# Kernel optimization log

Hardware: AMD Instinct MI355X
Metric: run time of the kernel (lower is better)

Reference implementation:

```python
import jax, jax.numpy as jnp
import numpy as np

EMBED_DIM = 512
NUM_HEADS = 8
QKV_DIM = 64
MS_HIDDEN = 16
COST_DIMS = 1
SCORES_DIMS = COST_DIMS + 1  # dot-product score + cost-mat score


def setup_inputs() -> dict:
    key = jax.random.key(0)
    ks = jax.random.split(key, 12)
    B, R, C = 8, 256, 256
    row_emb = jax.random.normal(ks[0], (B, R, EMBED_DIM), dtype=jnp.float32)
    col_emb = jax.random.normal(ks[1], (B, C, EMBED_DIM), dtype=jnp.float32)
    cost_mat = jax.random.uniform(ks[2], (B, R, C, COST_DIMS), dtype=jnp.float32)
    attn_mask = jax.random.randint(ks[3], (B, R, C), 0, 2).astype(jnp.bool_)
    # learned params (stored [in, out]; torch Linear applies x @ W.T)
    s = 1.0 / np.sqrt(EMBED_DIM)
    Wq = jax.random.uniform(ks[4], (EMBED_DIM, NUM_HEADS * QKV_DIM), minval=-s, maxval=s)
    Wk = jax.random.uniform(ks[5], (EMBED_DIM, NUM_HEADS * QKV_DIM), minval=-s, maxval=s)
    Wv = jax.random.uniform(ks[6], (EMBED_DIM, NUM_HEADS * QKV_DIM), minval=-s, maxval=s)
    Wo = jax.random.uniform(ks[7], (EMBED_DIM, EMBED_DIM), minval=-s, maxval=s)
    m1 = np.sqrt(1.0 / SCORES_DIMS)
    m2 = np.sqrt(1.0 / MS_HIDDEN)
    W1 = jax.random.uniform(ks[8], (SCORES_DIMS * NUM_HEADS, MS_HIDDEN * NUM_HEADS), minval=-m1, maxval=m1)
    W2 = jax.random.uniform(ks[9], (MS_HIDDEN * NUM_HEADS, NUM_HEADS), minval=-m2, maxval=m2)
    alpha = jnp.ones((1, NUM_HEADS, 1, 1, 1), dtype=jnp.float32)
    return {"row_emb": row_emb, "col_emb": col_emb, "cost_mat": cost_mat,
            "attn_mask": attn_mask, "Wq": Wq, "Wk": Wk, "Wv": Wv, "Wo": Wo,
            "W1": W1, "W2": W2, "alpha": alpha}


def reference(row_emb, col_emb, cost_mat, attn_mask, Wq, Wk, Wv, Wo, W1, W2, alpha):
    B, R, E = row_emb.shape
    C = col_emb.shape[1]
    H, D = NUM_HEADS, QKV_DIM
    norm = 1.0 / jnp.sqrt(jnp.asarray(D, row_emb.dtype))
    # projections -> (b, h, s, d)
    q = (row_emb @ Wq).reshape(B, R, H, D).transpose(0, 2, 1, 3)
    k = (col_emb @ Wk).reshape(B, C, H, D).transpose(0, 2, 1, 3)
    v = (col_emb @ Wv).reshape(B, C, H, D).transpose(0, 2, 1, 3)
    dot = norm * jnp.einsum('bhrd,bhcd->bhrc', q, k)  # (B,H,R,C)
    # mixed-score MLP: concat dot score with alpha-scaled cost-mat score
    cm = alpha * cost_mat[:, None]                    # (B,H,R,C,COST_DIMS)
    scores = jnp.concatenate([dot[..., None], cm], axis=-1)  # (B,H,R,C,S)
    s = scores.transpose(0, 2, 3, 1, 4).reshape(B, R, C, H * SCORES_DIMS)
    mixed = jax.nn.relu(s @ W1) @ W2                  # (B,R,C,H)
    logits = mixed.transpose(0, 3, 1, 2)              # (B,H,R,C)
    # masked softmax (rows fully masked -> zero weights)
    mask = attn_mask[:, None]                         # (B,1,R,C)
    all_masked = jnp.all(mask, axis=-1, keepdims=True)
    logits = jnp.where(mask, -jnp.inf, logits)
    weights = jax.nn.softmax(logits, axis=-1)
    weights = jnp.where(all_masked, 0.0, weights)
    out = jnp.einsum('bhrc,bhcd->bhrd', weights, v)   # (B,H,R,D)
    out = out.transpose(0, 2, 1, 3).reshape(B, R, H * D)
    return out @ Wo
```

## Files before the change

### kernel.cpp

```cpp
#include <hip/hip_runtime.h>
#include <hip/hip_bf16.h>

#define B_ 8
#define R_ 256
#define C_ 256
#define H_ 8
#define D_ 64

typedef __attribute__((ext_vector_type(8))) short s8v;
typedef __attribute__((ext_vector_type(4))) short s4v;
typedef __attribute__((ext_vector_type(4))) float f4v;

static __device__ __forceinline__ unsigned short f2b(float x) {
    __hip_bfloat16 h = __float2bfloat16(x);
    return *reinterpret_cast<unsigned short*>(&h);
}
static __device__ __forceinline__ float b2f(unsigned short u) {
    union { unsigned int i; float f; } c;
    c.i = (unsigned int)u << 16;
    return c.f;
}

__global__ __launch_bounds__(256) void prep(
    const float* __restrict__ re, const float* __restrict__ ce,
    const float* __restrict__ W1, const float* __restrict__ W2,
    const float* __restrict__ alpha,
    const float* __restrict__ Wq, const float* __restrict__ Wk,
    const float* __restrict__ Wv, const float* __restrict__ Wo,
    unsigned short* __restrict__ reb, unsigned short* __restrict__ ceb,
    unsigned short* __restrict__ w1af, unsigned short* __restrict__ w2af,
    unsigned short* __restrict__ wqt, unsigned short* __restrict__ wkt,
    unsigned short* __restrict__ wvt, unsigned short* __restrict__ wot)
{
    __shared__ unsigned short ldsT[64][68];
    if (blockIdx.x >= 2048) {
        const int bb = blockIdx.x - 2048;
        const int which = bb >> 6;
        const float* W = which == 0 ? Wq : which == 1 ? Wk : which == 2 ? Wv : Wo;
        unsigned short* WT = which == 0 ? wqt : which == 1 ? wkt : which == 2 ? wvt : wot;
        const int k0 = (bb & 7) * 64;
        const int n0 = ((bb >> 3) & 7) * 64;
        const int tt = threadIdx.x;
        const int rn = tt & 15;
        const int rk = tt >> 4;
        #pragma unroll
        for (int i = 0; i < 4; ++i) {
            const int kk = rk + 16 * i;
            const float4 v = *(const float4*)&W[(size_t)(k0 + kk) * 512 + n0 + rn * 4];
            ldsT[rn * 4 + 0][kk] = f2b(v.x);
            ldsT[rn * 4 + 1][kk] = f2b(v.y);
            ldsT[rn * 4 + 2][kk] = f2b(v.z);
            ldsT[rn * 4 + 3][kk] = f2b(v.w);
        }
        __syncthreads();
        #pragma unroll
        for (int i = 0; i < 4; ++i) {
            const int nn = rk + 16 * i;
            const s4v r = *(const s4v*)&ldsT[nn][rn * 4];
            *(s4v*)&WT[(size_t)(n0 + nn) * 512 + k0 + rn * 4] = r;
        }
        return;
    }

    const int t = blockIdx.x * 256 + threadIdx.x;
    {
        float2 v = *(const float2*)&re[(size_t)t * 2];
        reb[t * 2]     = f2b(v.x);
        reb[t * 2 + 1] = f2b(v.y);
        float2 w = *(const float2*)&ce[(size_t)t * 2];
        ceb[t * 2]     = f2b(w.x);
        ceb[t * 2 + 1] = f2b(w.y);
    }
    if (blockIdx.x == 0) {
        const int l = threadIdx.x;
        for (int q = 0; q < 16; ++q) {
            const int idx = l * 16 + q;
            const int kk = idx & 7, lane = (idx >> 3) & 63, n = idx >> 9;
            const int j = n * 16 + (lane & 15);
            const int s = 8 * (lane >> 4) + kk;
            float val = 0.f;
            if (s < 16) {
                val = W1[(2 * (s >> 1)) * 128 + j];
            } else if (s < 18) {
                for (int h = 0; h < 8; ++h)
                    val += alpha[h] * W1[(2 * h + 1) * 128 + j];
            }
            w1af[idx] = f2b(val);
        }
        for (int q = 0; q < 8; ++q) {
            const int idx = l * 8 + q;
            const int kk = idx & 7, lane = (idx >> 3) & 63, kc = idx >> 9;
            const int h = lane & 15, g = lane >> 4;
            const int phi = 16 * (2 * kc + (kk >> 2)) + 4 * g + (kk & 3);
            w2af[idx] = f2b(h < 8 ? W2[phi * 8 + h] : 0.f);
        }
    }
}

__global__ __launch_bounds__(256) void gemm_qkv(
    const unsigned short* __restrict__ reb, const unsigned short* __restrict__ ceb,
    const unsigned short* __restrict__ wqt, const unsigned short* __restrict__ wkt,
    const unsigned short* __restrict__ wvt,
    unsigned short* __restrict__ Qb, unsigned short* __restrict__ Kb,
    unsigned short* __restrict__ VT)
{
    const int z = blockIdx.z;
    const unsigned short* A;
    const unsigned short* Bm;
    int Ar0, Br0;
    if (z == 0)      { A = reb; Bm = wqt; Ar0 = blockIdx.x * 64; Br0 = blockIdx.y * 64; }
    else if (z == 1) { A = ceb; Bm = wkt; Ar0 = blockIdx.x * 64; Br0 = blockIdx.y * 64; }
    else             { A = wvt; Bm = ceb; Ar0 = blockIdx.y * 64; Br0 = blockIdx.x * 64; }

    const int t = threadIdx.x, lane = t & 63, wave = t >> 6;
    const int row0 = Ar0 + (wave >> 1) * 32;
    const int col0 = Br0 + (wave & 1) * 32;
    const int lr = lane & 15, ko = (lane >> 4) * 8;

    const unsigned short* Ap0 = A + (size_t)(row0 + lr) * 512 + ko;
    const unsigned short* Ap1 = Ap0 + 16 * 512;
    const unsigned short* Bp0 = Bm + (size_t)(col0 + lr) * 512 + ko;
    const unsigned short* Bp1 = Bp0 + 16 * 512;

    f4v acc[2][2] = {};
    #pragma unroll 4
    for (int k0 = 0; k0 < 512; k0 += 32) {
        s8v a0 = *(const s8v*)(Ap0 + k0);
        s8v a1 = *(const s8v*)(Ap1 + k0);
        s8v b0 = *(const s8v*)(Bp0 + k0);
        s8v b1 = *(const s8v*)(Bp1 + k0);
        acc[0][0] = __builtin_amdgcn_mfma_f32_16x16x32_bf16(a0, b0, acc[0][0], 0, 0, 0);
        acc[0][1] = __builtin_amdgcn_mfma_f32_16x16x32_bf16(a0, b1, acc[0][1], 0, 0, 0);
        acc[1][0] = __builtin_amdgcn_mfma_f32_16x16x32_bf16(a1, b0, acc[1][0], 0, 0, 0);
        acc[1][1] = __builtin_amdgcn_mfma_f32_16x16x32_bf16(a1, b1, acc[1][1], 0, 0, 0);
    }

    const float sc = (z == 0) ? 0.125f : 1.0f;
    const int rbase = (lane >> 4) * 4;
    #pragma unroll
    for (int i = 0; i < 2; ++i)
        #pragma unroll
        for (int j = 0; j < 2; ++j)
            #pragma unroll
            for (int reg = 0; reg < 4; ++reg) {
                const int rowIdx = row0 + i * 16 + rbase + reg;
                const int colIdx = col0 + j * 16 + lr;
                const unsigned short v = f2b(acc[i][j][reg] * sc);
                if (z == 0) {
                    Qb[(size_t)rowIdx * 512 + colIdx] = v;
                } else if (z == 1) {
                    const int b = rowIdx >> 8, c = rowIdx & 255;
                    const int h = colIdx >> 6, d = colIdx & 63;
                    Kb[(((size_t)b * 8 + h) * 256 + c) * 64 + d] = v;
                } else {
                    const int h = rowIdx >> 6, d = rowIdx & 63;
                    const int b = colIdx >> 8, c = colIdx & 255;
                    VT[(((size_t)b * 8 + h) * 64 + d) * 256 + c] = v;
                }
            }
}

__global__ __launch_bounds__(256) void gemm_out(
    const unsigned short* __restrict__ OHb, const unsigned short* __restrict__ wot,
    float* __restrict__ out)
{
    const int t = threadIdx.x, lane = t & 63, wave = t >> 6;
    const int row0 = blockIdx.x * 32 + (wave & 1) * 16;
    const int col0 = blockIdx.y * 64 + (wave >> 1) * 32;
    const int lr = lane & 15, ko = (lane >> 4) * 8;

    const unsigned short* Ap0 = OHb + (size_t)(row0 + lr) * 512 + ko;
    const unsigned short* Bp0 = wot + (size_t)(col0 + lr) * 512 + ko;
    const unsigned short* Bp1 = Bp0 + 16 * 512;

    f4v acc[2] = {};
    #pragma unroll 4
    for (int k0 = 0; k0 < 512; k0 += 32) {
        s8v a0 = *(const s8v*)(Ap0 + k0);
        s8v b0 = *(const s8v*)(Bp0 + k0);
        s8v b1 = *(const s8v*)(Bp1 + k0);
        acc[0] = __builtin_amdgcn_mfma_f32_16x16x32_bf16(a0, b0, acc[0], 0, 0, 0);
        acc[1] = __builtin_amdgcn_mfma_f32_16x16x32_bf16(a0, b1, acc[1], 0, 0, 0);
    }

    const int rbase = (lane >> 4) * 4;
    #pragma unroll
    for (int j = 0; j < 2; ++j)
        #pragma unroll
        for (int reg = 0; reg < 4; ++reg)
            out[(size_t)(row0 + rbase + reg) * 512 + col0 + j * 16 + lr] = acc[j][reg];
}

__global__ __launch_bounds__(512, 2) void attn_fused(
    const unsigned short* __restrict__ Qb,
    const unsigned short* __restrict__ Kb,
    const unsigned short* __restrict__ VT,
    const float* __restrict__ cost,
    const int* __restrict__ mask,
    const unsigned short* __restrict__ w1af,
    const unsigned short* __restrict__ w2af,
    unsigned short* __restrict__ OHb)
{
    __shared__ unsigned short dotb[4][256][24];
    __shared__ unsigned short w_t3[8][4][264];
    __shared__ unsigned short ws1[4096];
    __shared__ unsigned short ws2[2048];

    const int t    = threadIdx.x;
    const int lane = t & 63;
    const int w    = t >> 6;
    const int li   = lane & 15;
    const int g    = lane >> 4;
    const int b    = blockIdx.y;
    const int r0   = blockIdx.x * 4;

    ((s8v*)ws1)[t] = ((const s8v*)w1af)[t];
    if (t < 256) ((s8v*)ws2)[t] = ((const s8v*)w2af)[t];

    const int rB  = w & 3;
    const int ct0 = (w >> 2) * 8;
    float costv[8];
    {
        const float* costRow = cost + ((size_t)b * R_ + r0 + rB) * 256;
        #pragma unroll
        for (int i = 0; i < 8; ++i)
            costv[i] = costRow[(ct0 + i) * 16 + li];
    }
    int4 mk4[4];
    #pragma unroll
    for (int p = 0; p < 4; ++p) {
        const int idx = w * 4 + p;
        mk4[p] = *(const int4*)&mask[((size_t)b * R_ + r0 + (idx >> 3)) * 256 + lane * 4];
    }

    {
        const int rr = lane & 3;
        const int ko = g * 8;
        const unsigned short* Qp = Qb + ((size_t)b * R_ + r0 + rr) * 512 + w * 64 + ko;
        const s8v a0 = *(const s8v*)Qp;
        const s8v a1 = *(const s8v*)(Qp + 32);
        const unsigned short* Kp = Kb + (((size_t)b * 8 + w) * 256) * 64;
        #pragma unroll
        for (int ct = 0; ct < 16; ++ct) {
            const unsigned short* Bp = Kp + (size_t)(ct * 16 + li) * 64 + ko;
            const s8v b0 = *(const s8v*)Bp;
            const s8v b1v = *(const s8v*)(Bp + 32);
            f4v acc = __builtin_amdgcn_mfma_f32_16x16x32_bf16(a0, b0, (f4v){0.f,0.f,0.f,0.f}, 0, 0, 0);
            acc = __builtin_amdgcn_mfma_f32_16x16x32_bf16(a1, b1v, acc, 0, 0, 0);
            if (lane < 16) {
                const int c = ct * 16 + lane;
                #pragma unroll
                for (int reg = 0; reg < 4; ++reg) {
                    const float x = acc[reg];
                    const unsigned short hi = f2b(x);
                    const unsigned short lo = f2b(x - b2f(hi));
                    *(unsigned int*)&dotb[reg][c][2 * w] =
                        (unsigned int)hi | ((unsigned int)lo << 16);
                }
            }
        }
    }
    __syncthreads();

    {
        #pragma unroll
        for (int i = 0; i < 8; ++i) {
            const int c = (ct0 + i) * 16 + li;
            s8v b1;
            {
                const s8v t0 = *(const s8v*)&dotb[rB][c][(g & 1) * 8];
                const float cv = costv[i];
                const unsigned short chi = f2b(cv);
                const unsigned short clo = f2b(cv - b2f(chi));
                if (g < 2) {
                    b1 = t0;
                } else if (g == 2) {
                    s8v bc = {0, 0, 0, 0, 0, 0, 0, 0};
                    bc[0] = (short)chi; bc[1] = (short)clo;
                    b1 = bc;
                } else {
                    s8v bz = {0, 0, 0, 0, 0, 0, 0, 0};
                    b1 = bz;
                }
            }
            unsigned int pk[16];
            #pragma unroll
            for (int n = 0; n < 8; ++n) {
                const s8v w1A = *(const s8v*)&ws1[(n * 64 + lane) * 8];
                f4v acc = __builtin_amdgcn_mfma_f32_16x16x32_bf16(
                    w1A, b1, (f4v){0.f,0.f,0.f,0.f}, 0, 0, 0);
                const float a0 = fmaxf(acc[0], 0.f), a1 = fmaxf(acc[1], 0.f);
                const float a2 = fmaxf(acc[2], 0.f), a3 = fmaxf(acc[3], 0.f);
                pk[2 * n]     = (unsigned int)f2b(a0) | ((unsigned int)f2b(a1) << 16);
                pk[2 * n + 1] = (unsigned int)f2b(a2) | ((unsigned int)f2b(a3) << 16);
            }
            f4v acc2 = (f4v){0.f, 0.f, 0.f, 0.f};
            #pragma unroll
            for (int kc = 0; kc < 4; ++kc) {
                const s8v w2A = *(const s8v*)&ws2[(kc * 64 + lane) * 8];
                union { s8v v; unsigned int u[4]; } bb;
                bb.u[0] = pk[4 * kc + 0];
                bb.u[1] = pk[4 * kc + 1];
                bb.u[2] = pk[4 * kc + 2];
                bb.u[3] = pk[4 * kc + 3];
                acc2 = __builtin_amdgcn_mfma_f32_16x16x32_bf16(w2A, bb.v, acc2, 0, 0, 0);
            }
            if (g < 2) {
                float* lp = (float*)&dotb[rB][c][0];
                #pragma unroll
                for (int reg = 0; reg < 4; ++reg)
                    lp[4 * g + reg] = acc2[reg];
            }
        }
    }
    __syncthreads();

    {
        #pragma unroll
        for (int p = 0; p < 4; ++p) {
            const int idx = w * 4 + p;
            const int r = idx >> 3, h = idx & 7;
            const int4 mk = mk4[p];
            float v[4];
            #pragma unroll
            for (int i = 0; i < 4; ++i)
                v[i] = ((const float*)&dotb[r][lane * 4 + i][0])[h];
            const bool m0 = mk.x != 0, m1 = mk.y != 0;
            const bool m2 = mk.z != 0, m3 = mk.w != 0;
            const float v0 = m0 ? -INFINITY : v[0];
            const float v1 = m1 ? -INFINITY : v[1];
            const float v2 = m2 ? -INFINITY : v[2];
            const float v3 = m3 ? -INFINITY : v[3];
            float mx = fmaxf(fmaxf(v0, v1), fmaxf(v2, v3));
            #pragma unroll
            for (int off = 32; off >= 1; off >>= 1)
                mx = fmaxf(mx, __shfl_xor(mx, off));
            const float e0 = m0 ? 0.f : __expf(v0 - mx);
            const float e1 = m1 ? 0.f : __expf(v1 - mx);
            const float e2 = m2 ? 0.f : __expf(v2 - mx);
            const float e3 = m3 ? 0.f : __expf(v3 - mx);
            float sm = e0 + e1 + e2 + e3;
            #pragma unroll
            for (int off = 32; off >= 1; off >>= 1)
                sm += __shfl_xor(sm, off);
            const float inv = sm > 0.f ? 1.0f / sm : 0.f;
            s4v pk;
            pk[0] = (short)f2b(e0 * inv);
            pk[1] = (short)f2b(e1 * inv);
            pk[2] = (short)f2b(e2 * inv);
            pk[3] = (short)f2b(e3 * inv);
            *(s4v*)&w_t3[h][r][lane * 4] = pk;
        }
    }
    __syncthreads();

    {
        s8v bfr[8];
        #pragma unroll
        for (int kt = 0; kt < 8; ++kt)
            bfr[kt] = *(const s8v*)&w_t3[w][li & 3][kt * 32 + g * 8];
        const unsigned short* Vp = VT + (((size_t)b * 8 + w) * 64) * 256;
        #pragma unroll
        for (int dt = 0; dt < 4; ++dt) {
            const unsigned short* Ap = Vp + (size_t)(dt * 16 + li) * 256 + g * 8;
            f4v acc = (f4v){0.f, 0.f, 0.f, 0.f};
            #pragma unroll
            for (int kt = 0; kt < 8; ++kt)
                acc = __builtin_amdgcn_mfma_f32_16x16x32_bf16(
                    *(const s8v*)(Ap + kt * 32), bfr[kt], acc, 0, 0, 0);
            if (li < 4) {
                s4v o;
                o[0] = (short)f2b(acc[0]);
                o[1] = (short)f2b(acc[1]);
                o[2] = (short)f2b(acc[2]);
                o[3] = (short)f2b(acc[3]);
                *(s4v*)&OHb[((size_t)b * R_ + r0 + li) * 512 + w * 64 + dt * 16 + 4 * g] = o;
            }
        }
    }
}

extern "C" void kernel_launch(void* const* d_in, const int* in_sizes, int n_in,
                              void* d_out, int out_size, void* d_ws, size_t ws_size,
                              hipStream_t stream)
{
    const float* row_emb = (const float*)d_in[0];
    const float* col_emb = (const float*)d_in[1];
    const float* cost    = (const float*)d_in[2];
    const int*   mask    = (const int*)d_in[3];
    const float* Wq = (const float*)d_in[4];
    const float* Wk = (const float*)d_in[5];
    const float* Wv = (const float*)d_in[6];
    const float* Wo = (const float*)d_in[7];
    const float* W1 = (const float*)d_in[8];
    const float* W2 = (const float*)d_in[9];
    const float* alpha = (const float*)d_in[10];
    float* out = (float*)d_out;

    unsigned short* base = (unsigned short*)d_ws;
    unsigned short* Qb   = base;
    unsigned short* Kb   = base + 1048576;
    unsigned short* VT   = base + 2097152;
    unsigned short* OHb  = base + 3145728;
    unsigned short* reb  = base + 4194304;
    unsigned short* ceb  = base + 5242880;
    unsigned short* wqt  = base + 6291456;
    unsigned short* wkt  = base + 6553600;
    unsigned short* wvt  = base + 6815744;
    unsigned short* wot  = base + 7077888;
    unsigned short* w1af = base + 7340032;
    unsigned short* w2af = base + 7344128;

    prep<<<2304, 256, 0, stream>>>(row_emb, col_emb, W1, W2, alpha,
                                   Wq, Wk, Wv, Wo,
                                   reb, ceb, w1af, w2af, wqt, wkt, wvt, wot);
    gemm_qkv<<<dim3(32, 8, 3), 256, 0, stream>>>(reb, ceb, wqt, wkt, wvt,
                                                 Qb, Kb, VT);
    attn_fused<<<dim3(64, 8), 512, 0, stream>>>(Qb, Kb, VT, cost, mask,
                                                w1af, w2af, OHb);
    gemm_out<<<dim3(64, 8), 256, 0, stream>>>(OHb, wot, out);
}
```

Before: 91.60 us.

## Fuse fp32-to-bf16 embedding conversion into QKV GEMM and remap softmax mask layout

The separate prep pass that converted row and column embeddings to bf16 is removed. The QKV GEMM now loads the fp32 embeddings directly and converts them in registers before the MFMA, which saves a full write and re-read of the converted copies and shrinks the prep launch to the weight transposes only. The cost is that each GEMM block re-reads fp32 inputs (twice the bytes) and repeats the conversion for every column tile. The attention softmax also changes its work split: each wave now handles one row and four heads with strided, coalesced mask loads and scalar LDS stores, replacing the vectorised int4 mask loads and packed stores.

```diff
diff --git a/kernel.cpp b/kernel.cpp
--- a/kernel.cpp
+++ b/kernel.cpp
@@ -20,26 +20,35 @@
     c.i = (unsigned int)u << 16;
     return c.f;
 }
+static __device__ __forceinline__ s8v cvt8(const float* p) {
+    const float4 v0 = *(const float4*)p;
+    const float4 v1 = *(const float4*)(p + 4);
+    s8v r;
+    r[0] = (short)f2b(v0.x); r[1] = (short)f2b(v0.y);
+    r[2] = (short)f2b(v0.z); r[3] = (short)f2b(v0.w);
+    r[4] = (short)f2b(v1.x); r[5] = (short)f2b(v1.y);
+    r[6] = (short)f2b(v1.z); r[7] = (short)f2b(v1.w);
+    return r;
+}
 
 __global__ __launch_bounds__(256) void prep(
-    const float* __restrict__ re, const float* __restrict__ ce,
     const float* __restrict__ W1, const float* __restrict__ W2,
     const float* __restrict__ alpha,
     const float* __restrict__ Wq, const float* __restrict__ Wk,
     const float* __restrict__ Wv, const float* __restrict__ Wo,
-    unsigned short* __restrict__ reb, unsigned short* __restrict__ ceb,
     unsigned short* __restrict__ w1af, unsigned short* __restrict__ w2af,
     unsigned short* __restrict__ wqt, unsigned short* __restrict__ wkt,
     unsigned short* __restrict__ wvt, unsigned short* __restrict__ wot)
 {
     __shared__ unsigned short ldsT[64][68];
-    if (blockIdx.x >= 2048) {
-        const int bb = blockIdx.x - 2048;
+    if (blockIdx.x < 256) {
+        const int bb = blockIdx.x;
         const int which = bb >> 6;
         const float* W = which == 0 ? Wq : which == 1 ? Wk : which == 2 ? Wv : Wo;
         unsigned short* WT = which == 0 ? wqt : which == 1 ? wkt : which == 2 ? wvt : wot;
-        const int k0 = (bb & 7) * 64;
-        const int n0 = ((bb >> 3) & 7) * 64;
+        const int tile = bb & 63;
+        const int k0 = (tile & 7) * 64;
+        const int n0 = (tile >> 3) * 64;
         const int tt = threadIdx.x;
         const int rn = tt & 15;
         const int rk = tt >> 4;
@@ -61,17 +70,7 @@
         }
         return;
     }
-
-    const int t = blockIdx.x * 256 + threadIdx.x;
-    {
-        float2 v = *(const float2*)&re[(size_t)t * 2];
-        reb[t * 2]     = f2b(v.x);
-        reb[t * 2 + 1] = f2b(v.y);
-        float2 w = *(const float2*)&ce[(size_t)t * 2];
-        ceb[t * 2]     = f2b(w.x);
-        ceb[t * 2 + 1] = f2b(w.y);
-    }
-    if (blockIdx.x == 0) {
+    {
         const int l = threadIdx.x;
         for (int q = 0; q < 16; ++q) {
             const int idx = l * 16 + q;
@@ -98,41 +97,56 @@
 }
 
 __global__ __launch_bounds__(256) void gemm_qkv(
-    const unsigned short* __restrict__ reb, const unsigned short* __restrict__ ceb,
+    const float* __restrict__ re, const float* __restrict__ ce,
     const unsigned short* __restrict__ wqt, const unsigned short* __restrict__ wkt,
     const unsigned short* __restrict__ wvt,
     unsigned short* __restrict__ Qb, unsigned short* __restrict__ Kb,
     unsigned short* __restrict__ VT)
 {
     const int z = blockIdx.z;
-    const unsigned short* A;
-    const unsigned short* Bm;
+    const int t = threadIdx.x, lane = t & 63, wave = t >> 6;
     int Ar0, Br0;
-    if (z == 0)      { A = reb; Bm = wqt; Ar0 = blockIdx.x * 64; Br0 = blockIdx.y * 64; }
-    else if (z == 1) { A = ceb; Bm = wkt; Ar0 = blockIdx.x * 64; Br0 = blockIdx.y * 64; }
-    else             { A = wvt; Bm = ceb; Ar0 = blockIdx.y * 64; Br0 = blockIdx.x * 64; }
-
-    const int t = threadIdx.x, lane = t & 63, wave = t >> 6;
+    if (z == 2) { Ar0 = blockIdx.y * 64; Br0 = blockIdx.x * 64; }
+    else        { Ar0 = blockIdx.x * 64; Br0 = blockIdx.y * 64; }
     const int row0 = Ar0 + (wave >> 1) * 32;
     const int col0 = Br0 + (wave & 1) * 32;
     const int lr = lane & 15, ko = (lane >> 4) * 8;
 
-    const unsigned short* Ap0 = A + (size_t)(row0 + lr) * 512 + ko;
-    const unsigned short* Ap1 = Ap0 + 16 * 512;
-    const unsigned short* Bp0 = Bm + (size_t)(col0 + lr) * 512 + ko;
-    const unsigned short* Bp1 = Bp0 + 16 * 512;
-
     f4v acc[2][2] = {};
-    #pragma unroll 4
-    for (int k0 = 0; k0 < 512; k0 += 32) {
-        s8v a0 = *(const s8v*)(Ap0 + k0);
-        s8v a1 = *(const s8v*)(Ap1 + k0);
-        s8v b0 = *(const s8v*)(Bp0 + k0);
-        s8v b1 = *(const s8v*)(Bp1 + k0);
-        acc[0][0] = __builtin_amdgcn_mfma_f32_16x16x32_bf16(a0, b0, acc[0][0], 0, 0, 0);
-        acc[0][1] = __builtin_amdgcn_mfma_f32_16x16x32_bf16(a0, b1, acc[0][1], 0, 0, 0);
-        acc[1][0] = __builtin_amdgcn_mfma_f32_16x16x32_bf16(a1, b0, acc[1][0], 0, 0, 0);
-        acc[1][1] = __builtin_amdgcn_mfma_f32_16x16x32_bf16(a1, b1, acc[1][1], 0, 0, 0);
+    if (z < 2) {
+        const float* A32 = (z == 0) ? re : ce;
+        const unsigned short* Bw = (z == 0) ? wqt : wkt;
+        const float* Ap0 = A32 + (size_t)(row0 + lr) * 512 + ko;
+        const float* Ap1 = Ap0 + 16 * 512;
+        const unsigned short* Bp0 = Bw + (size_t)(col0 + lr) * 512 + ko;
+        const unsigned short* Bp1 = Bp0 + 16 * 512;
+        #pragma unroll 4
+        for (int k0 = 0; k0 < 512; k0 += 32) {
+            const s8v a0 = cvt8(Ap0 + k0);
+            const s8v a1 = cvt8(Ap1 + k0);
+            const s8v b0 = *(const s8v*)(Bp0 + k0);
+            const s8v b1 = *(const s8v*)(Bp1 + k0);
+            acc[0][0] = __builtin_amdgcn_mfma_f32_16x16x32_bf16(a0, b0, acc[0][0], 0, 0, 0);
+            acc[0][1] = __builtin_amdgcn_mfma_f32_16x16x32_bf16(a0, b1, acc[0][1], 0, 0, 0);
+            acc[1][0] = __builtin_amdgcn_mfma_f32_16x16x32_bf16(a1, b0, acc[1][0], 0, 0, 0);
+            acc[1][1] = __builtin_amdgcn_mfma_f32_16x16x32_bf16(a1, b1, acc[1][1], 0, 0, 0);
+        }
+    } else {
+        const unsigned short* Ap0 = wvt + (size_t)(row0 + lr) * 512 + ko;
+        const unsigned short* Ap1 = Ap0 + 16 * 512;
+        const float* Bp0 = ce + (size_t)(col0 + lr) * 512 + ko;
+        const float* Bp1 = Bp0 + 16 * 512;
+        #pragma unroll 4
+        for (int k0 = 0; k0 < 512; k0 += 32) {
+            const s8v a0 = *(const s8v*)(Ap0 + k0);
+            const s8v a1 = *(const s8v*)(Ap1 + k0);
+            const s8v b0 = cvt8(Bp0 + k0);
+            const s8v b1 = cvt8(Bp1 + k0);
+            acc[0][0] = __builtin_amdgcn_mfma_f32_16x16x32_bf16(a0, b0, acc[0][0], 0, 0, 0);
+            acc[0][1] = __builtin_amdgcn_mfma_f32_16x16x32_bf16(a0, b1, acc[0][1], 0, 0, 0);
+            acc[1][0] = __builtin_amdgcn_mfma_f32_16x16x32_bf16(a1, b0, acc[1][0], 0, 0, 0);
+            acc[1][1] = __builtin_amdgcn_mfma_f32_16x16x32_bf16(a1, b1, acc[1][1], 0, 0, 0);
+        }
     }
 
     const float sc = (z == 0) ? 0.125f : 1.0f;
@@ -226,11 +240,13 @@
         for (int i = 0; i < 8; ++i)
             costv[i] = costRow[(ct0 + i) * 16 + li];
     }
-    int4 mk4[4];
-    #pragma unroll
-    for (int p = 0; p < 4; ++p) {
-        const int idx = w * 4 + p;
-        mk4[p] = *(const int4*)&mask[((size_t)b * R_ + r0 + (idx >> 3)) * 256 + lane * 4];
+    const int rC = w >> 1;
+    int mkp[4];
+    {
+        const int* maskRow = mask + ((size_t)b * R_ + r0 + rC) * 256;
+        #pragma unroll
+        for (int i = 0; i < 4; ++i)
+            mkp[i] = maskRow[lane + 64 * i];
     }
 
     {
@@ -318,38 +334,33 @@
     {
         #pragma unroll
         for (int p = 0; p < 4; ++p) {
-            const int idx = w * 4 + p;
-            const int r = idx >> 3, h = idx & 7;
-            const int4 mk = mk4[p];
+            const int r = rC;
+            const int h = (w & 1) * 4 + p;
             float v[4];
             #pragma unroll
+            for (int i = 0; i < 4; ++i) {
+                const int c = lane + 64 * i;
+                v[i] = ((const float*)&dotb[r][c][0])[h];
+            }
+            #pragma unroll
             for (int i = 0; i < 4; ++i)
-                v[i] = ((const float*)&dotb[r][lane * 4 + i][0])[h];
-            const bool m0 = mk.x != 0, m1 = mk.y != 0;
-            const bool m2 = mk.z != 0, m3 = mk.w != 0;
-            const float v0 = m0 ? -INFINITY : v[0];
-            const float v1 = m1 ? -INFINITY : v[1];
-            const float v2 = m2 ? -INFINITY : v[2];
-            const float v3 = m3 ? -INFINITY : v[3];
-            float mx = fmaxf(fmaxf(v0, v1), fmaxf(v2, v3));
+                v[i] = mkp[i] ? -INFINITY : v[i];
+            float mx = fmaxf(fmaxf(v[0], v[1]), fmaxf(v[2], v[3]));
             #pragma unroll
             for (int off = 32; off >= 1; off >>= 1)
                 mx = fmaxf(mx, __shfl_xor(mx, off));
-            const float e0 = m0 ? 0.f : __expf(v0 - mx);
-            const float e1 = m1 ? 0.f : __expf(v1 - mx);
-            const float e2 = m2 ? 0.f : __expf(v2 - mx);
-            const float e3 = m3 ? 0.f : __expf(v3 - mx);
-            float sm = e0 + e1 + e2 + e3;
+            float e[4];
+            #pragma unroll
+            for (int i = 0; i < 4; ++i)
+                e[i] = mkp[i] ? 0.f : __expf(v[i] - mx);
+            float sm = e[0] + e[1] + e[2] + e[3];
             #pragma unroll
             for (int off = 32; off >= 1; off >>= 1)
                 sm += __shfl_xor(sm, off);
             const float inv = sm > 0.f ? 1.0f / sm : 0.f;
-            s4v pk;
-            pk[0] = (short)f2b(e0 * inv);
-            pk[1] = (short)f2b(e1 * inv);
-            pk[2] = (short)f2b(e2 * inv);
-            pk[3] = (short)f2b(e3 * inv);
-            *(s4v*)&w_t3[h][r][lane * 4] = pk;
+            #pragma unroll
+            for (int i = 0; i < 4; ++i)
+                w_t3[h][r][lane + 64 * i] = f2b(e[i] * inv);
         }
     }
     __syncthreads();
@@ -402,19 +413,16 @@
     unsigned short* Kb   = base + 1048576;
     unsigned short* VT   = base + 2097152;
     unsigned short* OHb  = base + 3145728;
-    unsigned short* reb  = base + 4194304;
-    unsigned short* ceb  = base + 5242880;
-    unsigned short* wqt  = base + 6291456;
-    unsigned short* wkt  = base + 6553600;
-    unsigned short* wvt  = base + 6815744;
-    unsigned short* wot  = base + 7077888;
-    unsigned short* w1af = base + 7340032;
-    unsigned short* w2af = base + 7344128;
-
-    prep<<<2304, 256, 0, stream>>>(row_emb, col_emb, W1, W2, alpha,
-                                   Wq, Wk, Wv, Wo,
-                                   reb, ceb, w1af, w2af, wqt, wkt, wvt, wot);
-    gemm_qkv<<<dim3(32, 8, 3), 256, 0, stream>>>(reb, ceb, wqt, wkt, wvt,
+    unsigned short* wqt  = base + 4194304;
+    unsigned short* wkt  = base + 4456448;
+    unsigned short* wvt  = base + 4718592;
+    unsigned short* wot  = base + 4980736;
+    unsigned short* w1af = base + 5242880;
+    unsigned short* w2af = base + 5246976;
+
+    prep<<<257, 256, 0, stream>>>(W1, W2, alpha, Wq, Wk, Wv, Wo,
+                                  w1af, w2af, wqt, wkt, wvt, wot);
+    gemm_qkv<<<dim3(32, 8, 3), 256, 0, stream>>>(row_emb, col_emb, wqt, wkt, wvt,
                                                  Qb, Kb, VT);
     attn_fused<<<dim3(64, 8), 512, 0, stream>>>(Qb, Kb, VT, cost, mask,
                                                 w1af, w2af, OHb);
```

New measurement: 101.8 us. 1.11x slower.

## Fuse output projection into attention kernel and keep MLP weights in registers

Applied to the files above, without the earlier changes.

Removes the separate gemm_out launch. Each attention block now multiplies its 4-row head outputs, staged in shared memory, against Wo and writes the fp32 result directly, so the OHb workspace round trip goes away. The mixed-score MLP weights are loaded into registers from global memory instead of being staged in LDS. The softmax is remapped so each wave handles one head across 4 rows, which drops a barrier. In exchange, every block rereads the full 512x512 Wo from L2, and register pressure rises under the 512-thread, 2-block launch bound.

```diff
diff --git a/kernel.cpp b/kernel.cpp
--- a/kernel.cpp
+++ b/kernel.cpp
@@ -160,37 +160,6 @@
             }
 }
 
-__global__ __launch_bounds__(256) void gemm_out(
-    const unsigned short* __restrict__ OHb, const unsigned short* __restrict__ wot,
-    float* __restrict__ out)
-{
-    const int t = threadIdx.x, lane = t & 63, wave = t >> 6;
-    const int row0 = blockIdx.x * 32 + (wave & 1) * 16;
-    const int col0 = blockIdx.y * 64 + (wave >> 1) * 32;
-    const int lr = lane & 15, ko = (lane >> 4) * 8;
-
-    const unsigned short* Ap0 = OHb + (size_t)(row0 + lr) * 512 + ko;
-    const unsigned short* Bp0 = wot + (size_t)(col0 + lr) * 512 + ko;
-    const unsigned short* Bp1 = Bp0 + 16 * 512;
-
-    f4v acc[2] = {};
-    #pragma unroll 4
-    for (int k0 = 0; k0 < 512; k0 += 32) {
-        s8v a0 = *(const s8v*)(Ap0 + k0);
-        s8v b0 = *(const s8v*)(Bp0 + k0);
-        s8v b1 = *(const s8v*)(Bp1 + k0);
-        acc[0] = __builtin_amdgcn_mfma_f32_16x16x32_bf16(a0, b0, acc[0], 0, 0, 0);
-        acc[1] = __builtin_amdgcn_mfma_f32_16x16x32_bf16(a0, b1, acc[1], 0, 0, 0);
-    }
-
-    const int rbase = (lane >> 4) * 4;
-    #pragma unroll
-    for (int j = 0; j < 2; ++j)
-        #pragma unroll
-        for (int reg = 0; reg < 4; ++reg)
-            out[(size_t)(row0 + rbase + reg) * 512 + col0 + j * 16 + lr] = acc[j][reg];
-}
-
 __global__ __launch_bounds__(512, 2) void attn_fused(
     const unsigned short* __restrict__ Qb,
     const unsigned short* __restrict__ Kb,
@@ -199,12 +168,12 @@
     const int* __restrict__ mask,
     const unsigned short* __restrict__ w1af,
     const unsigned short* __restrict__ w2af,
-    unsigned short* __restrict__ OHb)
+    const unsigned short* __restrict__ wot,
+    float* __restrict__ out)
 {
     __shared__ unsigned short dotb[4][256][24];
     __shared__ unsigned short w_t3[8][4][264];
-    __shared__ unsigned short ws1[4096];
-    __shared__ unsigned short ws2[2048];
+    __shared__ unsigned short ohs[4][520];
 
     const int t    = threadIdx.x;
     const int lane = t & 63;
@@ -214,9 +183,6 @@
     const int b    = blockIdx.y;
     const int r0   = blockIdx.x * 4;
 
-    ((s8v*)ws1)[t] = ((const s8v*)w1af)[t];
-    if (t < 256) ((s8v*)ws2)[t] = ((const s8v*)w2af)[t];
-
     const int rB  = w & 3;
     const int ct0 = (w >> 2) * 8;
     float costv[8];
@@ -226,11 +192,13 @@
         for (int i = 0; i < 8; ++i)
             costv[i] = costRow[(ct0 + i) * 16 + li];
     }
-    int4 mk4[4];
+    int mkp[4][4];
     #pragma unroll
-    for (int p = 0; p < 4; ++p) {
-        const int idx = w * 4 + p;
-        mk4[p] = *(const int4*)&mask[((size_t)b * R_ + r0 + (idx >> 3)) * 256 + lane * 4];
+    for (int r = 0; r < 4; ++r) {
+        const int* maskRow = mask + ((size_t)b * R_ + r0 + r) * 256;
+        #pragma unroll
+        for (int i = 0; i < 4; ++i)
+            mkp[r][i] = maskRow[lane + 64 * i];
     }
 
     {
@@ -263,6 +231,12 @@
     __syncthreads();
 
     {
+        s8v w1A[8], w2A[4];
+        #pragma unroll
+        for (int n = 0; n < 8; ++n) w1A[n] = ((const s8v*)w1af)[n * 64 + lane];
+        #pragma unroll
+        for (int kc = 0; kc < 4; ++kc) w2A[kc] = ((const s8v*)w2af)[kc * 64 + lane];
+
         #pragma unroll
         for (int i = 0; i < 8; ++i) {
             const int c = (ct0 + i) * 16 + li;
@@ -286,9 +260,8 @@
             unsigned int pk[16];
             #pragma unroll
             for (int n = 0; n < 8; ++n) {
-                const s8v w1A = *(const s8v*)&ws1[(n * 64 + lane) * 8];
                 f4v acc = __builtin_amdgcn_mfma_f32_16x16x32_bf16(
-                    w1A, b1, (f4v){0.f,0.f,0.f,0.f}, 0, 0, 0);
+                    w1A[n], b1, (f4v){0.f,0.f,0.f,0.f}, 0, 0, 0);
                 const float a0 = fmaxf(acc[0], 0.f), a1 = fmaxf(acc[1], 0.f);
                 const float a2 = fmaxf(acc[2], 0.f), a3 = fmaxf(acc[3], 0.f);
                 pk[2 * n]     = (unsigned int)f2b(a0) | ((unsigned int)f2b(a1) << 16);
@@ -297,13 +270,12 @@
             f4v acc2 = (f4v){0.f, 0.f, 0.f, 0.f};
             #pragma unroll
             for (int kc = 0; kc < 4; ++kc) {
-                const s8v w2A = *(const s8v*)&ws2[(kc * 64 + lane) * 8];
                 union { s8v v; unsigned int u[4]; } bb;
                 bb.u[0] = pk[4 * kc + 0];
                 bb.u[1] = pk[4 * kc + 1];
                 bb.u[2] = pk[4 * kc + 2];
                 bb.u[3] = pk[4 * kc + 3];
-                acc2 = __builtin_amdgcn_mfma_f32_16x16x32_bf16(w2A, bb.v, acc2, 0, 0, 0);
+                acc2 = __builtin_amdgcn_mfma_f32_16x16x32_bf16(w2A[kc], bb.v, acc2, 0, 0, 0);
             }
             if (g < 2) {
                 float* lp = (float*)&dotb[rB][c][0];
@@ -317,42 +289,32 @@
 
     {
         #pragma unroll
-        for (int p = 0; p < 4; ++p) {
-            const int idx = w * 4 + p;
-            const int r = idx >> 3, h = idx & 7;
-            const int4 mk = mk4[p];
+        for (int r = 0; r < 4; ++r) {
             float v[4];
             #pragma unroll
             for (int i = 0; i < 4; ++i)
-                v[i] = ((const float*)&dotb[r][lane * 4 + i][0])[h];
-            const bool m0 = mk.x != 0, m1 = mk.y != 0;
-            const bool m2 = mk.z != 0, m3 = mk.w != 0;
-            const float v0 = m0 ? -INFINITY : v[0];
-            const float v1 = m1 ? -INFINITY : v[1];
-            const float v2 = m2 ? -INFINITY : v[2];
-            const float v3 = m3 ? -INFINITY : v[3];
-            float mx = fmaxf(fmaxf(v0, v1), fmaxf(v2, v3));
+                v[i] = ((const float*)&dotb[r][lane + 64 * i][0])[w];
+            #pragma unroll
+            for (int i = 0; i < 4; ++i)
+                v[i] = mkp[r][i] ? -INFINITY : v[i];
+            float mx = fmaxf(fmaxf(v[0], v[1]), fmaxf(v[2], v[3]));
             #pragma unroll
             for (int off = 32; off >= 1; off >>= 1)
                 mx = fmaxf(mx, __shfl_xor(mx, off));
-            const float e0 = m0 ? 0.f : __expf(v0 - mx);
-            const float e1 = m1 ? 0.f : __expf(v1 - mx);
-            const float e2 = m2 ? 0.f : __expf(v2 - mx);
-            const float e3 = m3 ? 0.f : __expf(v3 - mx);
-            float sm = e0 + e1 + e2 + e3;
+            float e[4];
+            #pragma unroll
+            for (int i = 0; i < 4; ++i)
+                e[i] = mkp[r][i] ? 0.f : __expf(v[i] - mx);
+            float sm = e[0] + e[1] + e[2] + e[3];
             #pragma unroll
             for (int off = 32; off >= 1; off >>= 1)
                 sm += __shfl_xor(sm, off);
             const float inv = sm > 0.f ? 1.0f / sm : 0.f;
-            s4v pk;
-            pk[0] = (short)f2b(e0 * inv);
-            pk[1] = (short)f2b(e1 * inv);
-            pk[2] = (short)f2b(e2 * inv);
-            pk[3] = (short)f2b(e3 * inv);
-            *(s4v*)&w_t3[h][r][lane * 4] = pk;
-        }
-    }
-    __syncthreads();
+            #pragma unroll
+            for (int i = 0; i < 4; ++i)
+                w_t3[w][r][lane + 64 * i] = f2b(e[i] * inv);
+        }
+    }
 
     {
         s8v bfr[8];
@@ -374,8 +336,30 @@
                 o[1] = (short)f2b(acc[1]);
                 o[2] = (short)f2b(acc[2]);
                 o[3] = (short)f2b(acc[3]);
-                *(s4v*)&OHb[((size_t)b * R_ + r0 + li) * 512 + w * 64 + dt * 16 + 4 * g] = o;
-            }
+                *(s4v*)&ohs[li][w * 64 + dt * 16 + 4 * g] = o;
+            }
+        }
+    }
+    __syncthreads();
+
+    {
+        const int c0 = w * 64;
+        f4v acc[4] = {};
+        #pragma unroll
+        for (int kt = 0; kt < 16; ++kt) {
+            const s8v a = *(const s8v*)&ohs[lane & 3][kt * 32 + g * 8];
+            #pragma unroll
+            for (int dt = 0; dt < 4; ++dt) {
+                const s8v bv = *(const s8v*)&wot[(size_t)(c0 + dt * 16 + li) * 512 + kt * 32 + g * 8];
+                acc[dt] = __builtin_amdgcn_mfma_f32_16x16x32_bf16(a, bv, acc[dt], 0, 0, 0);
+            }
+        }
+        if (g == 0) {
+            #pragma unroll
+            for (int dt = 0; dt < 4; ++dt)
+                #pragma unroll
+                for (int reg = 0; reg < 4; ++reg)
+                    out[(size_t)(b * R_ + r0 + reg) * 512 + c0 + dt * 16 + li] = acc[dt][reg];
         }
     }
 }
@@ -401,15 +385,14 @@
     unsigned short* Qb   = base;
     unsigned short* Kb   = base + 1048576;
     unsigned short* VT   = base + 2097152;
-    unsigned short* OHb  = base + 3145728;
-    unsigned short* reb  = base + 4194304;
-    unsigned short* ceb  = base + 5242880;
-    unsigned short* wqt  = base + 6291456;
-    unsigned short* wkt  = base + 6553600;
-    unsigned short* wvt  = base + 6815744;
-    unsigned short* wot  = base + 7077888;
-    unsigned short* w1af = base + 7340032;
-    unsigned short* w2af = base + 7344128;
+    unsigned short* reb  = base + 3145728;
+    unsigned short* ceb  = base + 4194304;
+    unsigned short* wqt  = base + 5242880;
+    unsigned short* wkt  = base + 5505024;
+    unsigned short* wvt  = base + 5767168;
+    unsigned short* wot  = base + 6029312;
+    unsigned short* w1af = base + 6291456;
+    unsigned short* w2af = base + 6295552;
 
     prep<<<2304, 256, 0, stream>>>(row_emb, col_emb, W1, W2, alpha,
                                    Wq, Wk, Wv, Wo,
@@ -417,6 +400,5 @@
     gemm_qkv<<<dim3(32, 8, 3), 256, 0, stream>>>(reb, ceb, wqt, wkt, wvt,
                                                  Qb, Kb, VT);
     attn_fused<<<dim3(64, 8), 512, 0, stream>>>(Qb, Kb, VT, cost, mask,
-                                                w1af, w2af, OHb);
-    gemm_out<<<dim3(64, 8), 256, 0, stream>>>(OHb, wot, out);
-}
+                                                w1af, w2af, wot, out);
+}
```

New measurement: 106.5 us. 1.16x slower.

## Software-prefetch GEMM operands and remap softmax lanes to strided columns

Applied to the files above, without the earlier changes.

In the projection and output GEMMs, each loop iteration now loads the next k-slice of A/B operands into registers before issuing the MFMAs on the current slice, and the loop is fully unrolled, so global load latency can overlap with matrix math. In the fused attention kernel, the softmax phase changes its work split: each pair of waves handles one row, each wave covers four heads, and each lane handles columns lane+64*i instead of four contiguous columns. This lets each wave load mask values for a single row once, and the scalar LDS accesses on dotb and w_t3 get a different bank pattern. The cost is extra live registers from double-buffered operands and full unrolling, plus scalar 16-bit LDS stores that replace the earlier packed 64-bit store.

```diff
diff --git a/kernel.cpp b/kernel.cpp
--- a/kernel.cpp
+++ b/kernel.cpp
@@ -123,16 +123,23 @@
     const unsigned short* Bp1 = Bp0 + 16 * 512;
 
     f4v acc[2][2] = {};
-    #pragma unroll 4
+    s8v a0 = *(const s8v*)Ap0;
+    s8v a1 = *(const s8v*)Ap1;
+    s8v b0 = *(const s8v*)Bp0;
+    s8v b1 = *(const s8v*)Bp1;
+    #pragma unroll
     for (int k0 = 0; k0 < 512; k0 += 32) {
-        s8v a0 = *(const s8v*)(Ap0 + k0);
-        s8v a1 = *(const s8v*)(Ap1 + k0);
-        s8v b0 = *(const s8v*)(Bp0 + k0);
-        s8v b1 = *(const s8v*)(Bp1 + k0);
-        acc[0][0] = __builtin_amdgcn_mfma_f32_16x16x32_bf16(a0, b0, acc[0][0], 0, 0, 0);
-        acc[0][1] = __builtin_amdgcn_mfma_f32_16x16x32_bf16(a0, b1, acc[0][1], 0, 0, 0);
-        acc[1][0] = __builtin_amdgcn_mfma_f32_16x16x32_bf16(a1, b0, acc[1][0], 0, 0, 0);
-        acc[1][1] = __builtin_amdgcn_mfma_f32_16x16x32_bf16(a1, b1, acc[1][1], 0, 0, 0);
+        const s8v ca0 = a0, ca1 = a1, cb0 = b0, cb1 = b1;
+        if (k0 + 32 < 512) {
+            a0 = *(const s8v*)(Ap0 + k0 + 32);
+            a1 = *(const s8v*)(Ap1 + k0 + 32);
+            b0 = *(const s8v*)(Bp0 + k0 + 32);
+            b1 = *(const s8v*)(Bp1 + k0 + 32);
+        }
+        acc[0][0] = __builtin_amdgcn_mfma_f32_16x16x32_bf16(ca0, cb0, acc[0][0], 0, 0, 0);
+        acc[0][1] = __builtin_amdgcn_mfma_f32_16x16x32_bf16(ca0, cb1, acc[0][1], 0, 0, 0);
+        acc[1][0] = __builtin_amdgcn_mfma_f32_16x16x32_bf16(ca1, cb0, acc[1][0], 0, 0, 0);
+        acc[1][1] = __builtin_amdgcn_mfma_f32_16x16x32_bf16(ca1, cb1, acc[1][1], 0, 0, 0);
     }
 
     const float sc = (z == 0) ? 0.125f : 1.0f;
@@ -174,13 +181,19 @@
     const unsigned short* Bp1 = Bp0 + 16 * 512;
 
     f4v acc[2] = {};
-    #pragma unroll 4
+    s8v a0 = *(const s8v*)Ap0;
+    s8v b0 = *(const s8v*)Bp0;
+    s8v b1 = *(const s8v*)Bp1;
+    #pragma unroll
     for (int k0 = 0; k0 < 512; k0 += 32) {
-        s8v a0 = *(const s8v*)(Ap0 + k0);
-        s8v b0 = *(const s8v*)(Bp0 + k0);
-        s8v b1 = *(const s8v*)(Bp1 + k0);
-        acc[0] = __builtin_amdgcn_mfma_f32_16x16x32_bf16(a0, b0, acc[0], 0, 0, 0);
-        acc[1] = __builtin_amdgcn_mfma_f32_16x16x32_bf16(a0, b1, acc[1], 0, 0, 0);
+        const s8v ca0 = a0, cb0 = b0, cb1 = b1;
+        if (k0 + 32 < 512) {
+            a0 = *(const s8v*)(Ap0 + k0 + 32);
+            b0 = *(const s8v*)(Bp0 + k0 + 32);
+            b1 = *(const s8v*)(Bp1 + k0 + 32);
+        }
+        acc[0] = __builtin_amdgcn_mfma_f32_16x16x32_bf16(ca0, cb0, acc[0], 0, 0, 0);
+        acc[1] = __builtin_amdgcn_mfma_f32_16x16x32_bf16(ca0, cb1, acc[1], 0, 0, 0);
     }
 
     const int rbase = (lane >> 4) * 4;
@@ -226,11 +239,13 @@
         for (int i = 0; i < 8; ++i)
             costv[i] = costRow[(ct0 + i) * 16 + li];
     }
-    int4 mk4[4];
-    #pragma unroll
-    for (int p = 0; p < 4; ++p) {
-        const int idx = w * 4 + p;
-        mk4[p] = *(const int4*)&mask[((size_t)b * R_ + r0 + (idx >> 3)) * 256 + lane * 4];
+    const int rC = w >> 1;
+    int mkp[4];
+    {
+        const int* maskRow = mask + ((size_t)b * R_ + r0 + rC) * 256;
+        #pragma unroll
+        for (int i = 0; i < 4; ++i)
+            mkp[i] = maskRow[lane + 64 * i];
     }
 
     {
@@ -318,38 +333,33 @@
     {
         #pragma unroll
         for (int p = 0; p < 4; ++p) {
-            const int idx = w * 4 + p;
-            const int r = idx >> 3, h = idx & 7;
-            const int4 mk = mk4[p];
+            const int r = rC;
+            const int h = (w & 1) * 4 + p;
             float v[4];
             #pragma unroll
+            for (int i = 0; i < 4; ++i) {
+                const int c = lane + 64 * i;
+                v[i] = ((const float*)&dotb[r][c][0])[h];
+            }
+            #pragma unroll
             for (int i = 0; i < 4; ++i)
-                v[i] = ((const float*)&dotb[r][lane * 4 + i][0])[h];
-            const bool m0 = mk.x != 0, m1 = mk.y != 0;
-            const bool m2 = mk.z != 0, m3 = mk.w != 0;
-            const float v0 = m0 ? -INFINITY : v[0];
-            const float v1 = m1 ? -INFINITY : v[1];
-            const float v2 = m2 ? -INFINITY : v[2];
-            const float v3 = m3 ? -INFINITY : v[3];
-            float mx = fmaxf(fmaxf(v0, v1), fmaxf(v2, v3));
+                v[i] = mkp[i] ? -INFINITY : v[i];
+            float mx = fmaxf(fmaxf(v[0], v[1]), fmaxf(v[2], v[3]));
             #pragma unroll
             for (int off = 32; off >= 1; off >>= 1)
                 mx = fmaxf(mx, __shfl_xor(mx, off));
-            const float e0 = m0 ? 0.f : __expf(v0 - mx);
-            const float e1 = m1 ? 0.f : __expf(v1 - mx);
-            const float e2 = m2 ? 0.f : __expf(v2 - mx);
-            const float e3 = m3 ? 0.f : __expf(v3 - mx);
-            float sm = e0 + e1 + e2 + e3;
+            float e[4];
+            #pragma unroll
+            for (int i = 0; i < 4; ++i)
+                e[i] = mkp[i] ? 0.f : __expf(v[i] - mx);
+            float sm = e[0] + e[1] + e[2] + e[3];
             #pragma unroll
             for (int off = 32; off >= 1; off >>= 1)
                 sm += __shfl_xor(sm, off);
             const float inv = sm > 0.f ? 1.0f / sm : 0.f;
-            s4v pk;
-            pk[0] = (short)f2b(e0 * inv);
-            pk[1] = (short)f2b(e1 * inv);
-            pk[2] = (short)f2b(e2 * inv);
-            pk[3] = (short)f2b(e3 * inv);
-            *(s4v*)&w_t3[h][r][lane * 4] = pk;
+            #pragma unroll
+            for (int i = 0; i < 4; ++i)
+                w_t3[h][r][lane + 64 * i] = f2b(e[i] * inv);
         }
     }
     __syncthreads();
```

Result: no change. 91.44 us (-0.2%).
